# Optimization experiments

Measured on AMD Instinct MI355X. Metric: run time of the kernel, lower is better.

The kernel has to match this reference:

```python
import jax, jax.numpy as jnp
import numpy as np
import math

N, D, W, R = 131072, 128, 16, 5


def setup_inputs() -> dict:
    key = jax.random.key(0)
    k1, k2, k3, k4, k5 = jax.random.split(key, 5)
    stdv = 1.0 / math.sqrt(R)
    return {
        "embeds1": jax.random.normal(k1, (N, D), dtype=jnp.float32),
        "embeds2": jax.random.normal(k2, (N, D), dtype=jnp.float32),
        "rel_embeds": jax.random.normal(k3, (W, D * D), dtype=jnp.float32),
        "weight_scalars": jax.random.uniform(k4, (W, R), dtype=jnp.float32, minval=-stdv, maxval=stdv),
        "rels": jax.random.randint(k5, (N,), 0, R, dtype=jnp.int64),
    }


def reference(embeds1, embeds2, rel_embeds, weight_scalars, rels):
    n, d = embeds1.shape
    w, r = weight_scalars.shape
    rel_mats = rel_embeds.reshape(w, d, d)  # [W, D, D] per-basis bilinear matrices
    # basis_outputs[n, w] = embeds1[n] @ rel_mats[w] @ embeds2[n]
    basis_outputs = jnp.einsum('nd,wde,ne->nw', embeds1, rel_mats, embeds2)
    logit = basis_outputs @ weight_scalars            # [N, R]
    outputs = jax.nn.log_softmax(logit, axis=1)       # [N, R]
    # NLLLoss(mean) on log-probs gathered at the true relation
    log_probs = jnp.take_along_axis(outputs, rels[:, None], axis=1)  # [N, 1]
    loss = -log_probs.mean()
    # preds = sum_j (j+1) * p_j  (expected rating), shape [N, 1]
    ratings = jnp.arange(1, r + 1, dtype=outputs.dtype)
    preds = (jnp.exp(outputs) @ ratings)[:, None]
    return loss, preds
```

## Files before the change

### kernel.cpp

```cpp
#include <hip/hip_runtime.h>
#include <stdint.h>


#define NTOT 131072
#define DDIM 128
#define WBAS 16
#define RCLS 5
#define ROWS 32
#define WAVES 16
#define RPB  (WAVES * ROWS)
#define GRID2 (NTOT / RPB)
#define NTILE2 (NTOT / ROWS)

typedef __attribute__((ext_vector_type(8))) short bf16x8;
typedef __attribute__((ext_vector_type(4))) float f32x4;

__device__ __forceinline__ unsigned short f2bf(float x) {
    union { float f; unsigned u; } v; v.f = x;
    unsigned u = v.u + 0x7FFFu + ((v.u >> 16) & 1u);
    return (unsigned short)(u >> 16);
}

__device__ __forceinline__ ushort4 f2bf4(float4 v) {
    return make_ushort4(f2bf(v.x), f2bf(v.y), f2bf(v.z), f2bf(v.w));
}

__global__ __launch_bounds__(256) void prep_kernel(
    const float* __restrict__ rel_embeds,
    const float* __restrict__ wsc,
    unsigned short* __restrict__ Cth)
{
    __shared__ float tile[8][129];
    const int bx = blockIdx.x;
    const int r  = bx >> 4;
    const int d0 = (bx & 15) << 3;
    const int t  = threadIdx.x;

    const int e  = t & 127;
    const int dl = t >> 7;

    float acc[4] = {0.f, 0.f, 0.f, 0.f};
    for (int w = 0; w < WBAS; ++w) {
        float s = wsc[w * RCLS + r];
#pragma unroll
        for (int dd = 0; dd < 4; ++dd)
            acc[dd] += s * rel_embeds[w * 16384 + (d0 + dd * 2 + dl) * 128 + e];
    }
#pragma unroll
    for (int dd = 0; dd < 4; ++dd) tile[dd * 2 + dl][e] = acc[dd];
    __syncthreads();

    if (t < 128) {
        unsigned short h[8];
#pragma unroll
        for (int j = 0; j < 8; ++j) h[j] = f2bf(tile[j][t]);
        size_t base = (size_t)r * 16384 + (size_t)t * 128 + d0;
        *(ushort4*)(Cth + base)     = make_ushort4(h[0], h[1], h[2], h[3]);
        *(ushort4*)(Cth + base + 4) = make_ushort4(h[4], h[5], h[6], h[7]);
    }
}

#define PREF(buf, rr) do {                                                    \
    _Pragma("unroll")                                                         \
    for (int k4 = 0; k4 < 4; ++k4)                                            \
        buf[k4] = *(const bf16x8*)(rb + (rr) * 32768 + ((q * 16 + k4 * 64) ^ sw)); \
} while (0)

#define COMP(buf, rr) do {                                                    \
    f32x4 aa0 = {0.f,0.f,0.f,0.f}, ab0 = {0.f,0.f,0.f,0.f};                   \
    f32x4 aa1 = {0.f,0.f,0.f,0.f}, ab1 = {0.f,0.f,0.f,0.f};                   \
    aa0 = __builtin_amdgcn_mfma_f32_16x16x32_bf16(buf[0], bfr[0][0], aa0, 0, 0, 0); \
    aa1 = __builtin_amdgcn_mfma_f32_16x16x32_bf16(buf[0], bfr[1][0], aa1, 0, 0, 0); \
    ab0 = __builtin_amdgcn_mfma_f32_16x16x32_bf16(buf[2], bfr[0][2], ab0, 0, 0, 0); \
    ab1 = __builtin_amdgcn_mfma_f32_16x16x32_bf16(buf[2], bfr[1][2], ab1, 0, 0, 0); \
    aa0 = __builtin_amdgcn_mfma_f32_16x16x32_bf16(buf[1], bfr[0][1], aa0, 0, 0, 0); \
    aa1 = __builtin_amdgcn_mfma_f32_16x16x32_bf16(buf[1], bfr[1][1], aa1, 0, 0, 0); \
    ab0 = __builtin_amdgcn_mfma_f32_16x16x32_bf16(buf[3], bfr[0][3], ab0, 0, 0, 0); \
    ab1 = __builtin_amdgcn_mfma_f32_16x16x32_bf16(buf[3], bfr[1][3], ab1, 0, 0, 0); \
    f32x4 t0 = (aa0 + ab0) * e2a;                                             \
    f32x4 t1 = (aa1 + ab1) * e2b;                                             \
    s0[rr] += t0[0] + t0[1] + t0[2] + t0[3];                                  \
    s1[rr] += t1[0] + t1[1] + t1[2] + t1[3];                                  \
} while (0)

__global__ __launch_bounds__(1024, 2) void bilinear_mfma_kernel(
    const float* __restrict__ e1g,
    const float* __restrict__ e2g,
    const unsigned short* __restrict__ Cth,
    const int*   __restrict__ rels,
    float* __restrict__ out,
    float* __restrict__ loss_ws,
    float inv_n)
{
    __shared__ __align__(16) unsigned short s_c[81920];

    const int tid  = threadIdx.x;
    const int lane = tid & 63;
    const int w    = tid >> 6;
    const int l15  = lane & 15;
    const int q    = lane >> 4;

    const int n0 = blockIdx.x * RPB + w * ROWS;
    const int na = n0 + l15;
    const int nb = n0 + 16 + l15;

    bf16x8 bfr[2][4];
#pragma unroll
    for (int nt = 0; nt < 2; ++nt) {
        const float* p = e1g + (size_t)(n0 + 16 * nt + l15) * DDIM + q * 8;
#pragma unroll
        for (int k4 = 0; k4 < 4; ++k4) {
            float4 u0 = *(const float4*)(p + k4 * 32);
            float4 u1 = *(const float4*)(p + k4 * 32 + 4);
            union { ushort4 h[2]; bf16x8 v; } cv;
            cv.h[0] = f2bf4(u0);
            cv.h[1] = f2bf4(u1);
            bfr[nt][k4] = cv.v;
        }
    }

    const int rel0 = rels[na];
    const int rel1 = rels[nb];

#pragma unroll
    for (int j = 0; j < 10; ++j) {
        int gi = j * 1024 + tid;
        uint4 v = *(const uint4*)(Cth + gi * 8);
        int A  = gi * 16;
        int As = A ^ (((A >> 8) & 7) << 4);
        *(uint4*)((char*)s_c + As) = v;
    }

    __syncthreads();

    float s0[RCLS] = {0.f, 0.f, 0.f, 0.f, 0.f};
    float s1[RCLS] = {0.f, 0.f, 0.f, 0.f, 0.f};

    const int sw = (l15 & 7) << 4;
    const char* rowb = (const char*)s_c + l15 * 256;
    const float* e2pa = e2g + (size_t)na * DDIM + q * 4;
    const float* e2pb = e2g + (size_t)nb * DDIM + q * 4;

    f32x4 e2a = *(const f32x4*)(e2pa);
    f32x4 e2b = *(const f32x4*)(e2pb);

#pragma unroll 1
    for (int et = 0; et < 8; ++et) {
        const char* rb = rowb + et * 4096;

        bf16x8 afA[4], afB[4];
        PREF(afA, 0);

        f32x4 e2an, e2bn;
        if (et < 7) {
            e2an = *(const f32x4*)(e2pa + (et + 1) * 16);
            e2bn = *(const f32x4*)(e2pb + (et + 1) * 16);
        }

        PREF(afB, 1); COMP(afA, 0);
        PREF(afA, 2); COMP(afB, 1);
        PREF(afB, 3); COMP(afA, 2);
        PREF(afA, 4); COMP(afB, 3);
        COMP(afA, 4);

        e2a = e2an;
        e2b = e2bn;
    }

#pragma unroll
    for (int r = 0; r < RCLS; ++r) {
        s0[r] += __shfl_xor(s0[r], 16); s0[r] += __shfl_xor(s0[r], 32);
        s1[r] += __shfl_xor(s1[r], 16); s1[r] += __shfl_xor(s1[r], 32);
    }

    float m0 = s0[0], m1 = s1[0];
#pragma unroll
    for (int r = 1; r < RCLS; ++r) { m0 = fmaxf(m0, s0[r]); m1 = fmaxf(m1, s1[r]); }
    float se0 = 0.f, pn0 = 0.f, lr0 = 0.f;
    float se1 = 0.f, pn1 = 0.f, lr1 = 0.f;
#pragma unroll
    for (int r = 0; r < RCLS; ++r) {
        float e0 = __expf(s0[r] - m0);
        float e1v = __expf(s1[r] - m1);
        se0 += e0;  pn0 += (float)(r + 1) * e0;
        se1 += e1v; pn1 += (float)(r + 1) * e1v;
        if (r == rel0) lr0 = s0[r];
        if (r == rel1) lr1 = s1[r];
    }
    if (q == 0) {
        out[1 + na] = pn0 / se0;
        out[1 + nb] = pn1 / se1;
    }
    float lossc = (q == 0)
        ? -((lr0 - m0 - logf(se0)) + (lr1 - m1 - logf(se1))) * inv_n
        : 0.f;
#pragma unroll
    for (int mm = 1; mm <= 32; mm <<= 1) lossc += __shfl_xor(lossc, mm);
    if (lane == 0) loss_ws[blockIdx.x * WAVES + w] = lossc;
}

__global__ __launch_bounds__(256) void loss_reduce_kernel(
    const float* __restrict__ loss_ws, float* __restrict__ out)
{
    __shared__ float s[4];
    float v = 0.0f;
    for (int i = threadIdx.x; i < NTILE2; i += 256) v += loss_ws[i];
#pragma unroll
    for (int m = 1; m <= 32; m <<= 1) v += __shfl_xor(v, m);
    if ((threadIdx.x & 63) == 0) s[threadIdx.x >> 6] = v;
    __syncthreads();
    if (threadIdx.x == 0) out[0] = s[0] + s[1] + s[2] + s[3];
}

extern "C" void kernel_launch(void* const* d_in, const int* in_sizes, int n_in,
                              void* d_out, int out_size, void* d_ws, size_t ws_size,
                              hipStream_t stream) {
    const float* e1   = (const float*)d_in[0];
    const float* e2   = (const float*)d_in[1];
    const float* rele = (const float*)d_in[2];
    const float* wsc  = (const float*)d_in[3];
    const int*   rels = (const int*)d_in[4];
    float* out = (float*)d_out;

    unsigned short* Cth = (unsigned short*)d_ws;
    float* loss_ws = (float*)((char*)d_ws + 163840);

    prep_kernel<<<80, 256, 0, stream>>>(rele, wsc, Cth);
    bilinear_mfma_kernel<<<GRID2, 1024, 0, stream>>>(
        e1, e2, Cth, rels, out, loss_ws, 1.0f / (float)NTOT);
    loss_reduce_kernel<<<1, 256, 0, stream>>>(loss_ws, out);
}
```

Before: 172.5 us.

## Halve block size, keep two class matrices in LDS, stream the rest from global

Workgroups shrink from 16 to 8 waves. Only the first two of the five projected class matrices (64 KB) are staged in LDS; the other three are read per lane straight from global memory through the cache. This cuts the LDS footprint so more workgroups can be resident per CU, and the LDS staging is issued before the e1 fragment loads. MFMA sequences are wrapped in s_setprio, and the e2 prefetch across iterations is dropped. The trade-off is more L2/global traffic and more load latency inside the inner loop.

```diff
diff --git a/kernel.cpp b/kernel.cpp
--- a/kernel.cpp
+++ b/kernel.cpp
@@ -7,7 +7,7 @@
 #define WBAS 16
 #define RCLS 5
 #define ROWS 32
-#define WAVES 16
+#define WAVES 8
 #define RPB  (WAVES * ROWS)
 #define GRID2 (NTOT / RPB)
 #define NTILE2 (NTOT / ROWS)
@@ -66,9 +66,16 @@
         buf[k4] = *(const bf16x8*)(rb + (rr) * 32768 + ((q * 16 + k4 * 64) ^ sw)); \
 } while (0)
 
+#define GREF(buf, rr) do {                                                    \
+    _Pragma("unroll")                                                         \
+    for (int k4 = 0; k4 < 4; ++k4)                                            \
+        buf[k4] = *(const bf16x8*)(gb + (rr) * 16384 + k4 * 32);              \
+} while (0)
+
 #define COMP(buf, rr) do {                                                    \
     f32x4 aa0 = {0.f,0.f,0.f,0.f}, ab0 = {0.f,0.f,0.f,0.f};                   \
     f32x4 aa1 = {0.f,0.f,0.f,0.f}, ab1 = {0.f,0.f,0.f,0.f};                   \
+    __builtin_amdgcn_s_setprio(1);                                            \
     aa0 = __builtin_amdgcn_mfma_f32_16x16x32_bf16(buf[0], bfr[0][0], aa0, 0, 0, 0); \
     aa1 = __builtin_amdgcn_mfma_f32_16x16x32_bf16(buf[0], bfr[1][0], aa1, 0, 0, 0); \
     ab0 = __builtin_amdgcn_mfma_f32_16x16x32_bf16(buf[2], bfr[0][2], ab0, 0, 0, 0); \
@@ -77,13 +84,14 @@
     aa1 = __builtin_amdgcn_mfma_f32_16x16x32_bf16(buf[1], bfr[1][1], aa1, 0, 0, 0); \
     ab0 = __builtin_amdgcn_mfma_f32_16x16x32_bf16(buf[3], bfr[0][3], ab0, 0, 0, 0); \
     ab1 = __builtin_amdgcn_mfma_f32_16x16x32_bf16(buf[3], bfr[1][3], ab1, 0, 0, 0); \
+    __builtin_amdgcn_s_setprio(0);                                            \
     f32x4 t0 = (aa0 + ab0) * e2a;                                             \
     f32x4 t1 = (aa1 + ab1) * e2b;                                             \
     s0[rr] += t0[0] + t0[1] + t0[2] + t0[3];                                  \
     s1[rr] += t1[0] + t1[1] + t1[2] + t1[3];                                  \
 } while (0)
 
-__global__ __launch_bounds__(1024, 2) void bilinear_mfma_kernel(
+__global__ __launch_bounds__(512, 2) void bilinear_mfma_kernel(
     const float* __restrict__ e1g,
     const float* __restrict__ e2g,
     const unsigned short* __restrict__ Cth,
@@ -92,13 +100,22 @@
     float* __restrict__ loss_ws,
     float inv_n)
 {
-    __shared__ __align__(16) unsigned short s_c[81920];
+    __shared__ __align__(16) unsigned short s_c[32768];
 
     const int tid  = threadIdx.x;
     const int lane = tid & 63;
     const int w    = tid >> 6;
     const int l15  = lane & 15;
     const int q    = lane >> 4;
+
+#pragma unroll
+    for (int j = 0; j < 8; ++j) {
+        int gi = j * 512 + tid;
+        uint4 v = *(const uint4*)(Cth + gi * 8);
+        int A  = gi * 16;
+        int As = A ^ (((A >> 8) & 7) << 4);
+        *(uint4*)((char*)s_c + As) = v;
+    }
 
     const int n0 = blockIdx.x * RPB + w * ROWS;
     const int na = n0 + l15;
@@ -122,15 +139,6 @@
     const int rel0 = rels[na];
     const int rel1 = rels[nb];
 
-#pragma unroll
-    for (int j = 0; j < 10; ++j) {
-        int gi = j * 1024 + tid;
-        uint4 v = *(const uint4*)(Cth + gi * 8);
-        int A  = gi * 16;
-        int As = A ^ (((A >> 8) & 7) << 4);
-        *(uint4*)((char*)s_c + As) = v;
-    }
-
     __syncthreads();
 
     float s0[RCLS] = {0.f, 0.f, 0.f, 0.f, 0.f};
@@ -140,31 +148,29 @@
     const char* rowb = (const char*)s_c + l15 * 256;
     const float* e2pa = e2g + (size_t)na * DDIM + q * 4;
     const float* e2pb = e2g + (size_t)nb * DDIM + q * 4;
-
-    f32x4 e2a = *(const f32x4*)(e2pa);
-    f32x4 e2b = *(const f32x4*)(e2pb);
+    const unsigned short* gb0 = Cth + l15 * DDIM + q * 8;
 
 #pragma unroll 1
     for (int et = 0; et < 8; ++et) {
         const char* rb = rowb + et * 4096;
-
-        bf16x8 afA[4], afB[4];
+        const unsigned short* gb = gb0 + et * 2048;
+
+        bf16x8 afA[4], agA[4], agB[4];
+
+        GREF(agA, 2);
+        GREF(agB, 3);
+
+        f32x4 e2a = *(const f32x4*)(e2pa + et * 16);
+        f32x4 e2b = *(const f32x4*)(e2pb + et * 16);
+
         PREF(afA, 0);
-
-        f32x4 e2an, e2bn;
-        if (et < 7) {
-            e2an = *(const f32x4*)(e2pa + (et + 1) * 16);
-            e2bn = *(const f32x4*)(e2pb + (et + 1) * 16);
-        }
-
-        PREF(afB, 1); COMP(afA, 0);
-        PREF(afA, 2); COMP(afB, 1);
-        PREF(afB, 3); COMP(afA, 2);
-        PREF(afA, 4); COMP(afB, 3);
-        COMP(afA, 4);
-
-        e2a = e2an;
-        e2b = e2bn;
+        COMP(afA, 0);
+        PREF(afA, 1);
+        COMP(afA, 1);
+        COMP(agA, 2);
+        GREF(agA, 4);
+        COMP(agB, 3);
+        COMP(agA, 4);
     }
 
 #pragma unroll
@@ -226,7 +232,7 @@
     float* loss_ws = (float*)((char*)d_ws + 163840);
 
     prep_kernel<<<80, 256, 0, stream>>>(rele, wsc, Cth);
-    bilinear_mfma_kernel<<<GRID2, 1024, 0, stream>>>(
+    bilinear_mfma_kernel<<<GRID2, 512, 0, stream>>>(
         e1, e2, Cth, rels, out, loss_ws, 1.0f / (float)NTOT);
     loss_reduce_kernel<<<1, 256, 0, stream>>>(loss_ws, out);
 }
```

Result: slower. 195.5 us (+13.3%).
